# Kernel tuning notes

Hardware: AMD Instinct MI355X
Metric: run time of the kernel (lower is better)

The kernel has to match this reference:

```python
import jax, jax.numpy as jnp
import numpy as np

NUM_HEADS = 32
NUM_KV_HEADS = 8
HEAD_DIM = 128
SLIDING_WINDOW = 1024
ROPE_THETA = 10000.0


def _rotate_half(x):
    x1, x2 = jnp.split(x, 2, axis=-1)
    return jnp.concatenate((-x2, x1), axis=-1)


def _rope_cos_sin(seq_len, head_dim, theta, dtype):
    inv_freq = 1.0 / (theta ** (jnp.arange(0, head_dim, 2, dtype=jnp.float32) / head_dim))
    t = jnp.arange(seq_len, dtype=jnp.float32)
    freqs = t[:, None] * inv_freq[None, :]            # [S, hd/2]
    emb = jnp.concatenate((freqs, freqs), axis=-1)     # [S, hd]
    return jnp.cos(emb).astype(dtype), jnp.sin(emb).astype(dtype)


def setup_inputs() -> dict:
    key = jax.random.key(0)
    ks = jax.random.split(key, 5)
    B, S, H = 2, 2048, 4096
    kv_dim = NUM_KV_HEADS * HEAD_DIM
    scale = 1.0 / np.sqrt(H)
    return {
        "hidden_states": jax.random.normal(ks[0], (B, S, H), dtype=jnp.float32),
        "Wq": jax.random.normal(ks[1], (H, H), dtype=jnp.float32) * scale,
        "Wk": jax.random.normal(ks[2], (H, kv_dim), dtype=jnp.float32) * scale,
        "Wv": jax.random.normal(ks[3], (H, kv_dim), dtype=jnp.float32) * scale,
        "Wo": jax.random.normal(ks[4], (H, H), dtype=jnp.float32) * scale,
    }


def reference(hidden_states, Wq, Wk, Wv, Wo):
    B, S, H = hidden_states.shape
    groups = NUM_HEADS // NUM_KV_HEADS

    q = (hidden_states @ Wq).reshape(B, S, NUM_HEADS, HEAD_DIM).transpose(0, 2, 1, 3)
    k = (hidden_states @ Wk).reshape(B, S, NUM_KV_HEADS, HEAD_DIM).transpose(0, 2, 1, 3)
    v = (hidden_states @ Wv).reshape(B, S, NUM_KV_HEADS, HEAD_DIM).transpose(0, 2, 1, 3)

    cos, sin = _rope_cos_sin(S, HEAD_DIM, ROPE_THETA, q.dtype)  # [S, hd]
    q = q * cos + _rotate_half(q) * sin
    k = k * cos + _rotate_half(k) * sin

    # GQA: repeat_interleave kv heads to match query heads
    k = jnp.repeat(k, groups, axis=1)
    v = jnp.repeat(v, groups, axis=1)

    scores = jnp.einsum("bhqd,bhkd->bhqk", q, k) / np.sqrt(HEAD_DIM)

    i = jnp.arange(S)[:, None]
    j = jnp.arange(S)[None, :]
    allowed = (j <= i) & (i - j <= SLIDING_WINDOW // 2)  # causal + sliding window
    scores = jnp.where(allowed[None, None], scores, jnp.float32(-1e30))

    probs = jax.nn.softmax(scores, axis=-1)
    out = jnp.einsum("bhqk,bhkd->bhqd", probs, v)        # [B, nH, S, hd]
    out = out.transpose(0, 2, 1, 3).reshape(B, S, NUM_HEADS * HEAD_DIM)
    return out @ Wo
```

## Files before the change

### kernel.cpp

```cpp
#include <hip/hip_runtime.h>
#include <hip/hip_bf16.h>
#include <math.h>

#define BB 2
#define SS 2048
#define HH 4096
#define NH 32
#define NKV 8
#define HD 128
#define KVD (NKV*HD)
#define WIN 512
#define MROWS (BB*SS)

#define DT_BF16 1
#define DT_F32  2

typedef __hip_bfloat16 bf16;
typedef __attribute__((ext_vector_type(8))) short short8;
typedef __attribute__((ext_vector_type(4))) float f32x4;

__device__ __forceinline__ float ldf(const bf16* p){ return __bfloat162float(*p); }
__device__ __forceinline__ float ldf(const float* p){ return *p; }
__device__ __forceinline__ void stf(bf16* p, float v){ *p = __float2bfloat16(v); }
__device__ __forceinline__ void stf(float* p, float v){ *p = v; }

__global__ void detect_kernel(const void* __restrict__ w, int* __restrict__ flag)
{
  __shared__ int big;
  if (threadIdx.x == 0) big = 0;
  __syncthreads();
  const unsigned short* u = (const unsigned short*)w;
  for (int i = threadIdx.x; i < 2048; i += 256) {
    int ex = (u[i] >> 7) & 0xFF;
    if (ex >= 160) big = 1;
  }
  __syncthreads();
  if (threadIdx.x == 0) *flag = big ? DT_F32 : DT_BF16;
}

__global__ __launch_bounds__(256)
void cvt_x(const int* __restrict__ flag, const float* __restrict__ X,
           bf16* __restrict__ Y)
{
  if (*flag != DT_F32) return;
  const size_t idx = (size_t)blockIdx.x*256 + threadIdx.x;
  const f32x4 a = *(const f32x4*)(X + idx*8);
  const f32x4 b = *(const f32x4*)(X + idx*8 + 4);
  union { short8 s; bf16 h[8]; } u;
  #pragma unroll
  for (int j = 0; j < 4; j++) {
    u.h[j]     = __float2bfloat16(a[j]);
    u.h[j + 4] = __float2bfloat16(b[j]);
  }
  *(short8*)(Y + idx*8) = u.s;
}

template<typename TS>
__global__ __launch_bounds__(256)
void transpose_cvt(const int* __restrict__ flag, int mydt,
                   const TS* __restrict__ W0, const TS* __restrict__ W1,
                   bf16* __restrict__ D0, bf16* __restrict__ D1, int Kd, int Nd)
{
  if (*flag != mydt) return;
  const TS* W  = blockIdx.z ? W1 : W0;
  bf16*    WT  = blockIdx.z ? D1 : D0;
  __shared__ float tile[32][33];
  const int n0 = blockIdx.x*32, k0 = blockIdx.y*32;
  const int tx = threadIdx.x & 31, ty = threadIdx.x >> 5;
  #pragma unroll
  for (int j = 0; j < 4; j++)
    tile[ty + j*8][tx] = ldf(W + (size_t)(k0 + ty + j*8)*Nd + n0 + tx);
  __syncthreads();
  #pragma unroll
  for (int j = 0; j < 4; j++)
    WT[(size_t)(n0 + ty + j*8)*Kd + k0 + tx] = __float2bfloat16(tile[tx][ty + j*8]);
}

#define MFMA16(a,b,c) __builtin_amdgcn_mfma_f32_16x16x32_bf16(a,b,c,0,0,0)

template<typename TC>
__global__ __launch_bounds__(512)
void gemm256(const int* __restrict__ flag, int mydt,
             const bf16* __restrict__ A, const bf16* __restrict__ Bm,
             TC* __restrict__ C, int M, int N, int K)
{
  if (*flag != mydt) return;
  __shared__ __align__(16) bf16 lds[65536];
  const int tid = threadIdx.x;
  const int w = tid >> 6, lane = tid & 63;
  const int wm = w >> 2, wn = w & 3;
  const int fr = lane & 15, fq = lane >> 4;

  const int gx = gridDim.x;
  int wg = blockIdx.y*gx + blockIdx.x;
  const int cpx = (gx*gridDim.y) >> 3;
  wg = (wg & 7)*cpx + (wg >> 3);
  const int tM = (wg / gx)*256, tN = (wg % gx)*256;

  const int NT = K >> 6;

  auto stage = [&](int tt, int s){
    const int dbuf = tt & 1;
    const int hf = s & 1;
    const bf16* src = (s < 2) ? A : Bm;
    const int brow = ((s < 2) ? tM : tN) + hf*128;
    const int cbase = ((s < 2) ? 0 : 4096) + (dbuf*2 + hf)*1024;
    #pragma unroll
    for (int g = 0; g < 2; g++) {
      const int Ch = g*512 + tid;
      const int r = Ch >> 3, c = Ch & 7;
      const int cs = c ^ (r & 7);
      const bf16* gp = src + (size_t)(brow + r)*K + tt*64 + cs*8;
      char* lp = (char*)lds + (size_t)(cbase + g*512 + w*64)*16;
      __builtin_amdgcn_global_load_lds((const __attribute__((address_space(1))) void*)gp,
                                       (__attribute__((address_space(3))) void*)lp, 16, 0, 0);
    }
  };
  auto rdA = [&](int dbuf, int m, int kk) -> short8 {
    const int r = m*16 + fr;
    const int chunk = (dbuf*2 + wm)*1024 + r*8 + ((kk*4 + fq) ^ (r & 7));
    return *(const short8*)((char*)lds + (size_t)chunk*16);
  };
  auto rdB = [&](int dbuf, int n, int kk) -> short8 {
    const int rg = wn*64 + n*16 + fr;
    const int hf = rg >> 7, rr = rg & 127;
    const int chunk = 4096 + (dbuf*2 + hf)*1024 + rr*8 + ((kk*4 + fq) ^ (rr & 7));
    return *(const short8*)((char*)lds + (size_t)chunk*16);
  };

  f32x4 acc[8][4] = {};

  #pragma unroll
  for (int s = 0; s < 4; s++) stage(0, s);
  stage(1, 0); stage(1, 1);
  asm volatile("s_waitcnt vmcnt(4)" ::: "memory");
  __builtin_amdgcn_s_barrier();

  short8 a0[4][2], a1[4][2], b0[2][2], b1[2][2];
  for (int kt = 0; kt < NT; kt++) {
    const int db = kt & 1;
    #pragma unroll
    for (int m = 0; m < 4; m++){ a0[m][0]=rdA(db,m,0); a0[m][1]=rdA(db,m,1); }
    #pragma unroll
    for (int n = 0; n < 2; n++){ b0[n][0]=rdB(db,n,0); b0[n][1]=rdB(db,n,1); }
    if (kt+1 < NT) stage(kt+1, 2);
    asm volatile("s_waitcnt lgkmcnt(0)" ::: "memory");
    __builtin_amdgcn_sched_barrier(0);
    __builtin_amdgcn_s_setprio(1);
    #pragma unroll
    for (int m = 0; m < 4; m++)
      #pragma unroll
      for (int n = 0; n < 2; n++){
        acc[m][n] = MFMA16(a0[m][0], b0[n][0], acc[m][n]);
        acc[m][n] = MFMA16(a0[m][1], b0[n][1], acc[m][n]);
      }
    __builtin_amdgcn_s_setprio(0);
    __builtin_amdgcn_s_barrier();
    #pragma unroll
    for (int m = 0; m < 4; m++){ a1[m][0]=rdA(db,m+4,0); a1[m][1]=rdA(db,m+4,1); }
    #pragma unroll
    for (int n = 0; n < 2; n++){ b1[n][0]=rdB(db,n+2,0); b1[n][1]=rdB(db,n+2,1); }
    if (kt+1 < NT) stage(kt+1, 3);
    asm volatile("s_waitcnt lgkmcnt(0)" ::: "memory");
    __builtin_amdgcn_sched_barrier(0);
    __builtin_amdgcn_s_setprio(1);
    #pragma unroll
    for (int m = 0; m < 4; m++)
      #pragma unroll
      for (int n = 0; n < 2; n++){
        acc[m+4][n+2] = MFMA16(a1[m][0], b1[n][0], acc[m+4][n+2]);
        acc[m+4][n+2] = MFMA16(a1[m][1], b1[n][1], acc[m+4][n+2]);
      }
    __builtin_amdgcn_s_setprio(0);
    __builtin_amdgcn_s_barrier();
    if (kt+2 < NT) stage(kt+2, 0);
    __builtin_amdgcn_s_setprio(1);
    #pragma unroll
    for (int m = 0; m < 4; m++)
      #pragma unroll
      for (int n = 0; n < 2; n++){
        acc[m][n+2] = MFMA16(a0[m][0], b1[n][0], acc[m][n+2]);
        acc[m][n+2] = MFMA16(a0[m][1], b1[n][1], acc[m][n+2]);
      }
    __builtin_amdgcn_s_setprio(0);
    __builtin_amdgcn_s_barrier();
    if (kt+2 < NT) stage(kt+2, 1);
    __builtin_amdgcn_s_setprio(1);
    #pragma unroll
    for (int m = 0; m < 4; m++)
      #pragma unroll
      for (int n = 0; n < 2; n++){
        acc[m+4][n] = MFMA16(a1[m][0], b0[n][0], acc[m+4][n]);
        acc[m+4][n] = MFMA16(a1[m][1], b0[n][1], acc[m+4][n]);
      }
    __builtin_amdgcn_s_setprio(0);
    if (kt+2 < NT) { asm volatile("s_waitcnt vmcnt(4)" ::: "memory"); }
    else           { asm volatile("s_waitcnt vmcnt(0)" ::: "memory"); }
    __builtin_amdgcn_s_barrier();
  }

  #pragma unroll
  for (int m = 0; m < 8; m++)
    #pragma unroll
    for (int n = 0; n < 4; n++)
      #pragma unroll
      for (int r = 0; r < 4; r++)
        stf(C + (size_t)(tM + wm*128 + m*16 + fq*4 + r)*N + (tN + wn*64 + n*16 + fr),
            acc[m][n][r]);
}

__global__ __launch_bounds__(256)
void gemm_kv(const int* __restrict__ flag, int mydt, const bf16* __restrict__ A,
             const bf16* __restrict__ WTk, const bf16* __restrict__ WTv,
             bf16* __restrict__ Kout, bf16* __restrict__ VTout, int M, int N, int K)
{
  if (*flag != mydt) return;
  const bool vpath = blockIdx.z != 0;
  const bf16* Bm = vpath ? WTv : WTk;
  __shared__ __align__(16) bf16 As[128*32];
  __shared__ __align__(16) bf16 Bs[128*32];
  const int tid  = threadIdx.x;
  const int w    = tid >> 6;
  const int lane = tid & 63;
  const int wr = w >> 1, wc = w & 1;
  const int tM = blockIdx.y*128, tN = blockIdx.x*128;
  const int srow = tid >> 2;
  const int scol = (tid & 3) * 8;
  const int fr = lane & 15;
  const int kq = (lane >> 4) * 8;

  f32x4 acc[4][4] = {};

  for (int k0 = 0; k0 < K; k0 += 32) {
    __syncthreads();
    #pragma unroll
    for (int q = 0; q < 2; q++) {
      const int row = q*64 + srow;
      const bf16* ga = A  + (size_t)(tM + row)*K + k0 + scol;
      const bf16* gb = Bm + (size_t)(tN + row)*K + k0 + scol;
      char* la = (char*)As + q*4096 + w*1024;
      char* lb = (char*)Bs + q*4096 + w*1024;
      __builtin_amdgcn_global_load_lds((const __attribute__((address_space(1))) void*)ga,
                                       (__attribute__((address_space(3))) void*)la, 16, 0, 0);
      __builtin_amdgcn_global_load_lds((const __attribute__((address_space(1))) void*)gb,
                                       (__attribute__((address_space(3))) void*)lb, 16, 0, 0);
    }
    __syncthreads();

    short8 af[4], bfr[4];
    #pragma unroll
    for (int m = 0; m < 4; m++) af[m]  = *(const short8*)&As[(wr*64 + m*16 + fr)*32 + kq];
    #pragma unroll
    for (int n = 0; n < 4; n++) bfr[n] = *(const short8*)&Bs[(wc*64 + n*16 + fr)*32 + kq];
    #pragma unroll
    for (int m = 0; m < 4; m++)
      #pragma unroll
      for (int n = 0; n < 4; n++)
        acc[m][n] = MFMA16(af[m], bfr[n], acc[m][n]);
  }

  const int fq = lane >> 4;
  #pragma unroll
  for (int m = 0; m < 4; m++)
    #pragma unroll
    for (int n = 0; n < 4; n++)
      #pragma unroll
      for (int r = 0; r < 4; r++) {
        const int gm = tM + wr*64 + m*16 + fq*4 + r;
        const int gn = tN + wc*64 + n*16 + fr;
        if (vpath) {
          size_t idx = ((size_t)((gm >> 11)*NKV + (gn >> 7)))*((size_t)HD*SS)
                     + (size_t)(gn & 127)*SS + (gm & 2047);
          stf(VTout + idx, acc[m][n][r]);
        } else {
          stf(Kout + (size_t)gm*N + gn, acc[m][n][r]);
        }
      }
}

__global__ void rope_kernel(bf16* __restrict__ X, int nh)
{
  int idx = blockIdx.x*blockDim.x + threadIdx.x;
  int total = MROWS * nh * 64;
  if (idx >= total) return;
  int f   = idx & 63;
  int h   = (idx >> 6) % nh;
  int row = (idx >> 6) / nh;
  int s   = row & (SS - 1);
  float ang = (float)s * exp2f((float)f * -0.20762050593046014f);
  float sv, cv;
  __sincosf(ang, &sv, &cv);
  size_t base = (size_t)row*nh*HD + (size_t)h*HD;
  float x1 = ldf(X + base + f), x2 = ldf(X + base + 64 + f);
  stf(X + base + f,      x1*cv - x2*sv);
  stf(X + base + 64 + f, x2*cv + x1*sv);
}

__global__ __launch_bounds__(256, 2)
void attn_mfma(const bf16* __restrict__ Q, const bf16* __restrict__ K,
               const bf16* __restrict__ VT, bf16* __restrict__ Aout)
{
  int flat = (blockIdx.z*NH + blockIdx.y)*(SS/64) + blockIdx.x;
  flat = (flat & 7)*(BB*NH*(SS/64)/8) + (flat >> 3);
  const int i0 = (flat & 31) * 64;
  const int h  = (flat >> 5) & 31;
  const int b  = flat >> 10;
  const int kh = h >> 2;
  const int tid = threadIdx.x;
  const int w = tid >> 6, lane = tid & 63;
  const int fr = lane & 15, fq = lane >> 4;

  __shared__ __align__(16) bf16 Ks[64*128];
  __shared__ __align__(16) bf16 Vs[128*64];
  __shared__ __align__(16) bf16 Ps[4][16*64];

  const int qrow = w*16 + fr;
  const bf16* gq = Q + (size_t)(b*SS + i0 + qrow)*HH + h*HD + fq*8;
  short8 qf[4];
  #pragma unroll
  for (int kk = 0; kk < 4; kk++) qf[kk] = *(const short8*)(gq + kk*32);

  short8 kreg[4], vreg[4];
  auto loadKV = [&](int j0){
    const bf16* gk = K + (size_t)(b*SS + j0)*KVD + kh*HD;
    #pragma unroll
    for (int it = 0; it < 4; it++) {
      int slot = tid + it*256;
      int r = slot >> 4, cg = slot & 15;
      kreg[it] = *(const short8*)(gk + (size_t)r*KVD + cg*8);
    }
    const bf16* gv = VT + ((size_t)(b*NKV + kh)*HD)*SS + j0;
    #pragma unroll
    for (int it = 0; it < 4; it++) {
      int slot = tid + it*256;
      int d = slot >> 3, jg = slot & 7;
      vreg[it] = *(const short8*)(gv + (size_t)d*SS + jg*8);
    }
  };
  auto writeKV = [&](){
    #pragma unroll
    for (int it = 0; it < 4; it++) {
      int slot = tid + it*256;
      int r = slot >> 4, cg = slot & 15;
      *(short8*)((char*)Ks + r*256 + ((cg*16) ^ ((r & 7) << 4))) = kreg[it];
      int d = slot >> 3, jg = slot & 7;
      *(short8*)((char*)Vs + d*128 + ((jg*16) ^ ((d & 7) << 4))) = vreg[it];
    }
  };

  const float scale = 0.08838834764831845f;
  f32x4 o[8];
  #pragma unroll
  for (int nn = 0; nn < 8; nn++) o[nn] = (f32x4){0.f, 0.f, 0.f, 0.f};
  float m_run[4] = {-1e30f, -1e30f, -1e30f, -1e30f};
  float l_run[4] = {0.f, 0.f, 0.f, 0.f};

  const int j0_lo = (i0 >= WIN) ? (i0 - WIN) : 0;
  loadKV(j0_lo);

  for (int j0 = j0_lo; j0 <= i0; j0 += 64) {
    writeKV();
    __syncthreads();

    f32x4 sv[4];
    #pragma unroll
    for (int jf = 0; jf < 4; jf++) sv[jf] = (f32x4){0.f, 0.f, 0.f, 0.f};
    #pragma unroll
    for (int kk = 0; kk < 4; kk++) {
      #pragma unroll
      for (int jf = 0; jf < 4; jf++) {
        const int krow = jf*16 + fr;
        short8 kf = *(const short8*)((char*)Ks + krow*256 + ((kk*64 + fq*16) ^ ((krow & 7) << 4)));
        sv[jf] = MFMA16(qf[kk], kf, sv[jf]);
      }
    }

    if (j0 + 64 <= i0) loadKV(j0 + 64);

    const bool needmask = !((j0 >= i0 - 448) && (j0 <= i0 - 64));
    #pragma unroll
    for (int jf = 0; jf < 4; jf++)
      #pragma unroll
      for (int r = 0; r < 4; r++) {
        float x = sv[jf][r] * scale;
        if (needmask) {
          int iq = i0 + w*16 + fq*4 + r;
          int jv = j0 + jf*16 + fr;
          if (jv > iq || iq - jv > WIN) x = -1e30f;
        }
        sv[jf][r] = x;
      }

    float fac[4];
    #pragma unroll
    for (int r = 0; r < 4; r++) {
      float t = fmaxf(fmaxf(sv[0][r], sv[1][r]), fmaxf(sv[2][r], sv[3][r]));
      t = fmaxf(t, __shfl_xor(t, 1));
      t = fmaxf(t, __shfl_xor(t, 2));
      t = fmaxf(t, __shfl_xor(t, 4));
      t = fmaxf(t, __shfl_xor(t, 8));
      float mn = fmaxf(m_run[r], t);
      fac[r] = __expf(m_run[r] - mn);
      m_run[r] = mn;
    }
    #pragma unroll
    for (int r = 0; r < 4; r++) {
      float sum = 0.f;
      #pragma unroll
      for (int jf = 0; jf < 4; jf++) {
        float p = __expf(sv[jf][r] - m_run[r]);
        sv[jf][r] = p;
        sum += p;
      }
      sum += __shfl_xor(sum, 1);
      sum += __shfl_xor(sum, 2);
      sum += __shfl_xor(sum, 4);
      sum += __shfl_xor(sum, 8);
      l_run[r] = l_run[r]*fac[r] + sum;
    }

    char* pbase = (char*)(&Ps[w][0]);
    #pragma unroll
    for (int jf = 0; jf < 4; jf++)
      #pragma unroll
      for (int r = 0; r < 4; r++) {
        int q = fq*4 + r, j = jf*16 + fr;
        *(bf16*)(pbase + q*128 + ((j*2) ^ ((q & 7) << 4))) = __float2bfloat16(sv[jf][r]);
      }

    #pragma unroll
    for (int nn = 0; nn < 8; nn++)
      #pragma unroll
      for (int r = 0; r < 4; r++) o[nn][r] *= fac[r];

    #pragma unroll
    for (int kt = 0; kt < 2; kt++) {
      short8 ap = *(const short8*)(pbase + fr*128 + ((kt*64 + fq*16) ^ ((fr & 7) << 4)));
      #pragma unroll
      for (int nn = 0; nn < 8; nn++) {
        const int d = nn*16 + fr;
        short8 vf = *(const short8*)((char*)Vs + d*128 + ((kt*64 + fq*16) ^ ((d & 7) << 4)));
        o[nn] = MFMA16(ap, vf, o[nn]);
      }
    }
    __syncthreads();
  }

  float inv[4];
  #pragma unroll
  for (int r = 0; r < 4; r++) inv[r] = 1.0f / l_run[r];
  bf16* ao = Aout + (size_t)(b*SS + i0 + w*16)*HH + h*HD;
  #pragma unroll
  for (int nn = 0; nn < 8; nn++)
    #pragma unroll
    for (int r = 0; r < 4; r++)
      stf(ao + (size_t)(fq*4 + r)*HH + nn*16 + fr, o[nn][r] * inv[r]);
}

extern "C" void kernel_launch(void* const* d_in, const int* in_sizes, int n_in,
                              void* d_out, int out_size, void* d_ws, size_t ws_size,
                              hipStream_t stream)
{
  char* ws = (char*)d_ws;
  const size_t MB = (size_t)1 << 20;
  int*  flag = (int*)ws;
  bf16* Q  = (bf16*)(ws + 256);
  bf16* K  = (bf16*)(ws + 256 + 32*MB);
  bf16* VT = (bf16*)(ws + 256 + 40*MB);
  bf16* S  = (bf16*)(ws + 256 + 48*MB);
  bf16* WTk = S;
  bf16* WTv = S + (size_t)KVD*HH;
  bf16* WTo = Q;
  bf16* Xb = (bf16*)d_out;

  detect_kernel<<<1, 256, 0, stream>>>(d_in[1], flag);
  cvt_x<<<MROWS*HH/8/256, 256, 0, stream>>>(flag, (const float*)d_in[0], Xb);

  auto tr1 = [&](const void* W, int Kd, int Nd, bf16* dst){
    dim3 g(Nd/32, Kd/32, 1);
    transpose_cvt<bf16 ><<<g,256,0,stream>>>(flag, DT_BF16, (const bf16 *)W, (const bf16 *)W, dst, dst, Kd, Nd);
    transpose_cvt<float><<<g,256,0,stream>>>(flag, DT_F32 , (const float*)W, (const float*)W, dst, dst, Kd, Nd);
  };

  tr1(d_in[1], HH, HH, S);
  {
    dim3 g(HH/256, MROWS/256);
    gemm256<bf16><<<g,512,0,stream>>>(flag, DT_BF16, (const bf16*)d_in[0], S, Q, MROWS, HH, HH);
    gemm256<bf16><<<g,512,0,stream>>>(flag, DT_F32 , Xb,                   S, Q, MROWS, HH, HH);
  }
  {
    dim3 gt(KVD/32, HH/32, 2);
    transpose_cvt<bf16 ><<<gt,256,0,stream>>>(flag, DT_BF16, (const bf16 *)d_in[2], (const bf16 *)d_in[3], WTk, WTv, HH, KVD);
    transpose_cvt<float><<<gt,256,0,stream>>>(flag, DT_F32 , (const float*)d_in[2], (const float*)d_in[3], WTk, WTv, HH, KVD);
    dim3 g(KVD/128, MROWS/128, 2);
    gemm_kv<<<g,256,0,stream>>>(flag, DT_BF16, (const bf16*)d_in[0], WTk, WTv, K, VT, MROWS, KVD, HH);
    gemm_kv<<<g,256,0,stream>>>(flag, DT_F32 , Xb,                   WTk, WTv, K, VT, MROWS, KVD, HH);
  }

  rope_kernel<<<(MROWS*NH *64 + 255)/256, 256, 0, stream>>>(Q, NH);
  rope_kernel<<<(MROWS*NKV*64 + 255)/256, 256, 0, stream>>>(K, NKV);
  attn_mfma<<<dim3(SS/64, NH, BB), 256, 0, stream>>>(Q, K, VT, S);

  tr1(d_in[4], HH, HH, WTo);
  {
    dim3 g(HH/256, MROWS/256);
    gemm256<bf16 ><<<g,512,0,stream>>>(flag, DT_BF16, S, WTo, (bf16 *)d_out, MROWS, HH, HH);
    gemm256<float><<<g,512,0,stream>>>(flag, DT_F32 , S, WTo, (float*)d_out, MROWS, HH, HH);
  }
}
```

Before: 705.5 us.

## Merge dtype-dispatched kernel pairs and prefetch second LDS fragment set earlier

Each pair of bf16/f32 launches for transpose, Q/O GEMM and KV GEMM becomes a single launch that picks the input pointer or output dtype at runtime from the flag. This removes the early-exit dummy launches and their launch overhead. In the main GEMM loop, the second half's LDS fragment reads and the global stage are now issued before the first MFMA block, with a partial lgkmcnt wait and one barrier removed, so LDS latency overlaps with MFMA work. Keeping both fragment sets live at once raises register pressure, and dropping the barrier could risk a hazard on LDS buffer reuse.

```diff
diff --git a/kernel.cpp b/kernel.cpp
--- a/kernel.cpp
+++ b/kernel.cpp
@@ -55,21 +55,23 @@
   *(short8*)(Y + idx*8) = u.s;
 }
 
-template<typename TS>
 __global__ __launch_bounds__(256)
-void transpose_cvt(const int* __restrict__ flag, int mydt,
-                   const TS* __restrict__ W0, const TS* __restrict__ W1,
-                   bf16* __restrict__ D0, bf16* __restrict__ D1, int Kd, int Nd)
-{
-  if (*flag != mydt) return;
-  const TS* W  = blockIdx.z ? W1 : W0;
-  bf16*    WT  = blockIdx.z ? D1 : D0;
+void transpose_cvt(const int* __restrict__ flag,
+                   const void* W0, const void* W1,
+                   bf16* D0, bf16* D1, int Kd, int Nd)
+{
+  const bool isf32 = (*flag == DT_F32);
+  const void* W = blockIdx.z ? W1 : W0;
+  bf16*     WT  = blockIdx.z ? D1 : D0;
   __shared__ float tile[32][33];
   const int n0 = blockIdx.x*32, k0 = blockIdx.y*32;
   const int tx = threadIdx.x & 31, ty = threadIdx.x >> 5;
   #pragma unroll
-  for (int j = 0; j < 4; j++)
-    tile[ty + j*8][tx] = ldf(W + (size_t)(k0 + ty + j*8)*Nd + n0 + tx);
+  for (int j = 0; j < 4; j++) {
+    const size_t off = (size_t)(k0 + ty + j*8)*Nd + n0 + tx;
+    tile[ty + j*8][tx] = isf32 ? ((const float*)W)[off]
+                               : __bfloat162float(((const bf16*)W)[off]);
+  }
   __syncthreads();
   #pragma unroll
   for (int j = 0; j < 4; j++)
@@ -78,13 +80,15 @@
 
 #define MFMA16(a,b,c) __builtin_amdgcn_mfma_f32_16x16x32_bf16(a,b,c,0,0,0)
 
-template<typename TC>
+template<int OUTF>
 __global__ __launch_bounds__(512)
-void gemm256(const int* __restrict__ flag, int mydt,
-             const bf16* __restrict__ A, const bf16* __restrict__ Bm,
-             TC* __restrict__ C, int M, int N, int K)
-{
-  if (*flag != mydt) return;
+void gemm256(const int* __restrict__ flag,
+             const bf16* __restrict__ Abf, const bf16* __restrict__ Axb,
+             const bf16* __restrict__ Bm, void* __restrict__ C,
+             int M, int N, int K)
+{
+  const bool isf32 = (*flag == DT_F32);
+  const bf16* A = isf32 ? Axb : Abf;
   __shared__ __align__(16) bf16 lds[65536];
   const int tid = threadIdx.x;
   const int w = tid >> 6, lane = tid & 63;
@@ -144,7 +148,13 @@
     #pragma unroll
     for (int n = 0; n < 2; n++){ b0[n][0]=rdB(db,n,0); b0[n][1]=rdB(db,n,1); }
     if (kt+1 < NT) stage(kt+1, 2);
-    asm volatile("s_waitcnt lgkmcnt(0)" ::: "memory");
+    __builtin_amdgcn_sched_barrier(0);
+    #pragma unroll
+    for (int m = 0; m < 4; m++){ a1[m][0]=rdA(db,m+4,0); a1[m][1]=rdA(db,m+4,1); }
+    #pragma unroll
+    for (int n = 0; n < 2; n++){ b1[n][0]=rdB(db,n+2,0); b1[n][1]=rdB(db,n+2,1); }
+    if (kt+1 < NT) stage(kt+1, 3);
+    asm volatile("s_waitcnt lgkmcnt(12)" ::: "memory");
     __builtin_amdgcn_sched_barrier(0);
     __builtin_amdgcn_s_setprio(1);
     #pragma unroll
@@ -155,12 +165,6 @@
         acc[m][n] = MFMA16(a0[m][1], b0[n][1], acc[m][n]);
       }
     __builtin_amdgcn_s_setprio(0);
-    __builtin_amdgcn_s_barrier();
-    #pragma unroll
-    for (int m = 0; m < 4; m++){ a1[m][0]=rdA(db,m+4,0); a1[m][1]=rdA(db,m+4,1); }
-    #pragma unroll
-    for (int n = 0; n < 2; n++){ b1[n][0]=rdB(db,n+2,0); b1[n][1]=rdB(db,n+2,1); }
-    if (kt+1 < NT) stage(kt+1, 3);
     asm volatile("s_waitcnt lgkmcnt(0)" ::: "memory");
     __builtin_amdgcn_sched_barrier(0);
     __builtin_amdgcn_s_setprio(1);
@@ -204,17 +208,21 @@
     #pragma unroll
     for (int n = 0; n < 4; n++)
       #pragma unroll
-      for (int r = 0; r < 4; r++)
-        stf(C + (size_t)(tM + wm*128 + m*16 + fq*4 + r)*N + (tN + wn*64 + n*16 + fr),
-            acc[m][n][r]);
+      for (int r = 0; r < 4; r++) {
+        const size_t off = (size_t)(tM + wm*128 + m*16 + fq*4 + r)*N
+                         + (tN + wn*64 + n*16 + fr);
+        if (OUTF && isf32) ((float*)C)[off] = acc[m][n][r];
+        else               stf((bf16*)C + off, acc[m][n][r]);
+      }
 }
 
 __global__ __launch_bounds__(256)
-void gemm_kv(const int* __restrict__ flag, int mydt, const bf16* __restrict__ A,
+void gemm_kv(const int* __restrict__ flag,
+             const bf16* __restrict__ Abf, const bf16* __restrict__ Axb,
              const bf16* __restrict__ WTk, const bf16* __restrict__ WTv,
              bf16* __restrict__ Kout, bf16* __restrict__ VTout, int M, int N, int K)
 {
-  if (*flag != mydt) return;
+  const bf16* A = (*flag == DT_F32) ? Axb : Abf;
   const bool vpath = blockIdx.z != 0;
   const bf16* Bm = vpath ? WTv : WTk;
   __shared__ __align__(16) bf16 As[128*32];
@@ -472,39 +480,21 @@
   bf16* WTv = S + (size_t)KVD*HH;
   bf16* WTo = Q;
   bf16* Xb = (bf16*)d_out;
+  const bf16* X0 = (const bf16*)d_in[0];
 
   detect_kernel<<<1, 256, 0, stream>>>(d_in[1], flag);
   cvt_x<<<MROWS*HH/8/256, 256, 0, stream>>>(flag, (const float*)d_in[0], Xb);
 
-  auto tr1 = [&](const void* W, int Kd, int Nd, bf16* dst){
-    dim3 g(Nd/32, Kd/32, 1);
-    transpose_cvt<bf16 ><<<g,256,0,stream>>>(flag, DT_BF16, (const bf16 *)W, (const bf16 *)W, dst, dst, Kd, Nd);
-    transpose_cvt<float><<<g,256,0,stream>>>(flag, DT_F32 , (const float*)W, (const float*)W, dst, dst, Kd, Nd);
-  };
-
-  tr1(d_in[1], HH, HH, S);
-  {
-    dim3 g(HH/256, MROWS/256);
-    gemm256<bf16><<<g,512,0,stream>>>(flag, DT_BF16, (const bf16*)d_in[0], S, Q, MROWS, HH, HH);
-    gemm256<bf16><<<g,512,0,stream>>>(flag, DT_F32 , Xb,                   S, Q, MROWS, HH, HH);
-  }
-  {
-    dim3 gt(KVD/32, HH/32, 2);
-    transpose_cvt<bf16 ><<<gt,256,0,stream>>>(flag, DT_BF16, (const bf16 *)d_in[2], (const bf16 *)d_in[3], WTk, WTv, HH, KVD);
-    transpose_cvt<float><<<gt,256,0,stream>>>(flag, DT_F32 , (const float*)d_in[2], (const float*)d_in[3], WTk, WTv, HH, KVD);
-    dim3 g(KVD/128, MROWS/128, 2);
-    gemm_kv<<<g,256,0,stream>>>(flag, DT_BF16, (const bf16*)d_in[0], WTk, WTv, K, VT, MROWS, KVD, HH);
-    gemm_kv<<<g,256,0,stream>>>(flag, DT_F32 , Xb,                   WTk, WTv, K, VT, MROWS, KVD, HH);
-  }
+  transpose_cvt<<<dim3(HH/32, HH/32, 1), 256, 0, stream>>>(flag, d_in[1], d_in[1], S, S, HH, HH);
+  gemm256<0><<<dim3(HH/256, MROWS/256), 512, 0, stream>>>(flag, X0, Xb, S, Q, MROWS, HH, HH);
+
+  transpose_cvt<<<dim3(KVD/32, HH/32, 2), 256, 0, stream>>>(flag, d_in[2], d_in[3], WTk, WTv, HH, KVD);
+  gemm_kv<<<dim3(KVD/128, MROWS/128, 2), 256, 0, stream>>>(flag, X0, Xb, WTk, WTv, K, VT, MROWS, KVD, HH);
 
   rope_kernel<<<(MROWS*NH *64 + 255)/256, 256, 0, stream>>>(Q, NH);
   rope_kernel<<<(MROWS*NKV*64 + 255)/256, 256, 0, stream>>>(K, NKV);
   attn_mfma<<<dim3(SS/64, NH, BB), 256, 0, stream>>>(Q, K, VT, S);
 
-  tr1(d_in[4], HH, HH, WTo);
-  {
-    dim3 g(HH/256, MROWS/256);
-    gemm256<bf16 ><<<g,512,0,stream>>>(flag, DT_BF16, S, WTo, (bf16 *)d_out, MROWS, HH, HH);
-    gemm256<float><<<g,512,0,stream>>>(flag, DT_F32 , S, WTo, (float*)d_out, MROWS, HH, HH);
-  }
-}
+  transpose_cvt<<<dim3(HH/32, HH/32, 1), 256, 0, stream>>>(flag, d_in[4], d_in[4], WTo, WTo, HH, HH);
+  gemm256<1><<<dim3(HH/256, MROWS/256), 512, 0, stream>>>(flag, S, S, WTo, d_out, MROWS, HH, HH);
+}
```

Result: no change. 718.3 us (+1.8%).
